# Optimization experiments

Measured on AMD Instinct MI355X. Metric: run time of the kernel, lower is better.

## Reference

```python
import jax, jax.numpy as jnp
import numpy as np

B, P, C = 64, 8732, 81
NEG_POS_RATIO = 3


def _smooth_l1_masked_sum(p, t, maskf):
    # smooth_l1 with beta=1, sum reduction, restricted to positive priors
    d = jnp.abs(p - t)
    l = jnp.where(d < 1.0, 0.5 * d * d, d - 0.5)  # [B,P,K]
    return jnp.sum(l.sum(-1) * maskf)


def setup_inputs() -> dict:
    key = jax.random.key(0)
    ks = jax.random.split(key, 6)
    loc_data = jax.random.normal(ks[0], (B, P, 4), jnp.float32)
    conf_data = jax.random.normal(ks[1], (B, P, C), jnp.float32)
    four_corners_data = jax.random.normal(ks[2], (B, P, 8), jnp.float32)
    loc_t = jax.random.normal(ks[3], (B, P, 4), jnp.float32)
    four_corners_t = jax.random.normal(ks[4], (B, P, 8), jnp.float32)
    conf_t = jax.random.randint(ks[5], (B, P), 0, C, jnp.int32)
    return {
        "loc_data": loc_data,
        "conf_data": conf_data,
        "four_corners_data": four_corners_data,
        "loc_t": loc_t,
        "four_corners_t": four_corners_t,
        "conf_t": conf_t,
    }


def reference(loc_data, conf_data, four_corners_data, loc_t, four_corners_t, conf_t):
    num_priors = conf_data.shape[1]
    pos = conf_t > 0                                  # [B,P]
    posf = pos.astype(conf_data.dtype)

    # localization + four-corner smooth-L1 over matched (positive) priors
    loss_l = _smooth_l1_masked_sum(loc_data, loc_t, posf)
    loss_four_corners = _smooth_l1_masked_sum(four_corners_data, four_corners_t, posf)

    # per-prior CE loss: log_sum_exp(conf) - conf[target]
    lse = jax.nn.logsumexp(conf_data, axis=-1)        # [B,P]
    gathered = jnp.take_along_axis(conf_data, conf_t[..., None], axis=-1)[..., 0]
    ce_all = lse - gathered                           # [B,P]

    # hard-negative mining: rank negatives by CE loss (double argsort)
    loss_c_mine = jnp.where(pos, 0.0, ce_all)
    loss_idx = jnp.argsort(-loss_c_mine, axis=1)      # descending sort indices
    idx_rank = jnp.argsort(loss_idx, axis=1)          # rank of each prior
    num_pos = pos.sum(axis=1, keepdims=True)          # [B,1]
    num_neg = jnp.minimum(NEG_POS_RATIO * num_pos, num_priors - 1)
    neg = idx_rank < num_neg                          # [B,P]

    sel = pos | neg
    loss_c = jnp.sum(jnp.where(sel, ce_all, 0.0))

    N = num_pos.sum().astype(conf_data.dtype)
    return (loss_l / N, loss_c / N, loss_four_corners / N)
```

## Files before the change

kernel.cpp:

```cpp
#include <hip/hip_runtime.h>


#define NB 64
#define NP 8732
#define NC 81
constexpr int BP = NB * NP;
constexpr int PBLK = (NP + 255) / 256;

__device__ inline float sl1(float d) {
    d = fabsf(d);
    return d < 1.0f ? 0.5f * d * d : d - 0.5f;
}

__global__ void k_init(float* acc_area) {
    if (threadIdx.x < 194) acc_area[threadIdx.x] = 0.0f;
}

__global__ __launch_bounds__(256) void k_main(
    const float* __restrict__ loc_data, const float* __restrict__ conf_data,
    const float* __restrict__ fc_data,  const float* __restrict__ loc_t,
    const float* __restrict__ fc_t,     const int* __restrict__ conf_t,
    float* __restrict__ ce, float* __restrict__ acc,
    int* __restrict__ npos_b, float* __restrict__ spos_b, float* __restrict__ sneg_b)
{
    const int b = blockIdx.y;
    const int t = threadIdx.x;
    const int p = (blockIdx.x << 8) + t;

    float l_sum = 0.0f, f_sum = 0.0f, sp = 0.0f, sn = 0.0f;
    int np = 0;

    if (p < NP) {
        const size_t g = (size_t)b * NP + p;
        const int tgt = conf_t[g];
        const float posf = (tgt > 0) ? 1.0f : 0.0f;
        np = (tgt > 0) ? 1 : 0;

        float4 a  = ((const float4*)loc_data)[g];
        float4 at = ((const float4*)loc_t)[g];
        l_sum = (sl1(a.x - at.x) + sl1(a.y - at.y) +
                 sl1(a.z - at.z) + sl1(a.w - at.w)) * posf;
        float4 c0 = ((const float4*)fc_data)[2 * g];
        float4 c1 = ((const float4*)fc_data)[2 * g + 1];
        float4 d0 = ((const float4*)fc_t)[2 * g];
        float4 d1 = ((const float4*)fc_t)[2 * g + 1];
        f_sum = (sl1(c0.x - d0.x) + sl1(c0.y - d0.y) + sl1(c0.z - d0.z) + sl1(c0.w - d0.w) +
                 sl1(c1.x - d1.x) + sl1(c1.y - d1.y) + sl1(c1.z - d1.z) + sl1(c1.w - d1.w)) * posf;

        const float* row = conf_data + g * NC;
        float s0 = 0.0f, s1 = 0.0f, s2 = 0.0f, s3 = 0.0f;
        #pragma unroll 5
        for (int c = 0; c < 80; c += 4) {
            s0 += __expf(row[c]);
            s1 += __expf(row[c + 1]);
            s2 += __expf(row[c + 2]);
            s3 += __expf(row[c + 3]);
        }
        float s = (s0 + s1) + (s2 + s3) + __expf(row[80]);
        float cev = __logf(s) - row[tgt];
        ce[g] = cev;
        sp = cev * posf;
        sn = cev - sp;
    }

    __shared__ float red[4][5];
    const int wave = t >> 6, lane = t & 63;
    float vnp = (float)np;
    #pragma unroll
    for (int o = 32; o; o >>= 1) {
        l_sum += __shfl_xor(l_sum, o, 64);
        f_sum += __shfl_xor(f_sum, o, 64);
        sp    += __shfl_xor(sp, o, 64);
        sn    += __shfl_xor(sn, o, 64);
        vnp   += __shfl_xor(vnp, o, 64);
    }
    if (lane == 0) {
        red[wave][0] = l_sum; red[wave][1] = f_sum;
        red[wave][2] = sp;    red[wave][3] = sn;   red[wave][4] = vnp;
    }
    __syncthreads();
    if (t == 0) {
        float rl = 0, rf = 0, rp = 0, rn = 0, rc = 0;
        #pragma unroll
        for (int w = 0; w < 4; ++w) {
            rl += red[w][0]; rf += red[w][1]; rp += red[w][2];
            rn += red[w][3]; rc += red[w][4];
        }
        atomicAdd(&acc[0], rl);
        atomicAdd(&acc[1], rf);
        atomicAdd(&spos_b[b], rp);
        atomicAdd(&sneg_b[b], rn);
        atomicAdd(&npos_b[b], (int)rc);
    }
}

__global__ __launch_bounds__(256) void k_batch(
    const float* __restrict__ ce, const int* __restrict__ conf_t,
    const int* __restrict__ npos_b, const float* __restrict__ spos_b,
    const float* __restrict__ sneg_b, float* __restrict__ loss_c_b)
{
    const int b = blockIdx.x;
    const int t = threadIdx.x;
    const int npos    = npos_b[b];
    const int nneg    = NP - npos;
    const int num_neg = min(3 * npos, NP - 1);

    if (num_neg >= nneg) {
        if (t == 0) loss_c_b[b] = spos_b[b] + sneg_b[b];
        return;
    }
    if (num_neg <= 0) {
        if (t == 0) loss_c_b[b] = spos_b[b];
        return;
    }

    __shared__ float ce_s[NP];
    __shared__ float sredf[4];
    __shared__ int   sredi[4];
    const float* crow = ce + (size_t)b * NP;
    const int*   trow = conf_t + (size_t)b * NP;
    for (int p = t; p < NP; p += 256)
        ce_s[p] = (trow[p] > 0) ? -1.0f : crow[p];
    __syncthreads();

    const int wave = t >> 6, lane = t & 63;
    const int K = num_neg;
    unsigned lo = 0u, hi = 0x7f800000u;
    while (lo < hi) {
        unsigned mid = lo + ((hi - lo) >> 1);
        float v = __uint_as_float(mid);
        int c_t = 0;
        for (int p = t; p < NP; p += 256) c_t += (ce_s[p] > v) ? 1 : 0;
        #pragma unroll
        for (int o = 32; o; o >>= 1) c_t += __shfl_xor(c_t, o, 64);
        __syncthreads();
        if (lane == 0) sredi[wave] = c_t;
        __syncthreads();
        int cnt = sredi[0] + sredi[1] + sredi[2] + sredi[3];
        if (cnt < K) hi = mid; else lo = mid + 1;
    }
    float v = __uint_as_float(lo);
    int c_t = 0; float s_t = 0.0f;
    for (int p = t; p < NP; p += 256) {
        float x = ce_s[p];
        if (x > v) { c_t++; s_t += x; }
    }
    #pragma unroll
    for (int o = 32; o; o >>= 1) {
        c_t += __shfl_xor(c_t, o, 64);
        s_t += __shfl_xor(s_t, o, 64);
    }
    __syncthreads();
    if (lane == 0) { sredi[wave] = c_t; sredf[wave] = s_t; }
    __syncthreads();
    if (t == 0) {
        int   cnt = sredi[0] + sredi[1] + sredi[2] + sredi[3];
        float sgt = sredf[0] + sredf[1] + sredf[2] + sredf[3];
        loss_c_b[b] = spos_b[b] + sgt + (float)(K - cnt) * v;
    }
}

__global__ void k_final(const float* __restrict__ acc,
                        const float* __restrict__ loss_c_b,
                        const int* __restrict__ npos_b,
                        float* __restrict__ out)
{
    const int t = threadIdx.x;
    float lc = loss_c_b[t];
    int   np = npos_b[t];
    #pragma unroll
    for (int o = 32; o; o >>= 1) {
        lc += __shfl_xor(lc, o, 64);
        np += __shfl_xor(np, o, 64);
    }
    if (t == 0) {
        float N = (float)np;
        out[0] = acc[0] / N;
        out[1] = lc / N;
        out[2] = acc[1] / N;
    }
}

extern "C" void kernel_launch(void* const* d_in, const int* in_sizes, int n_in,
                              void* d_out, int out_size, void* d_ws, size_t ws_size,
                              hipStream_t stream)
{
    const float* loc_data  = (const float*)d_in[0];
    const float* conf_data = (const float*)d_in[1];
    const float* fc_data   = (const float*)d_in[2];
    const float* loc_t     = (const float*)d_in[3];
    const float* fc_t      = (const float*)d_in[4];
    const int*   conf_t    = (const int*)d_in[5];
    float* out = (float*)d_out;

    float* ce       = (float*)d_ws;
    float* acc      = ce + BP;
    int*   npos_b   = (int*)(acc + 2);
    float* spos_b   = (float*)(npos_b + 64);
    float* sneg_b   = spos_b + 64;
    float* loss_c_b = sneg_b + 64;

    hipLaunchKernelGGL(k_init,  dim3(1), dim3(256), 0, stream, acc);
    hipLaunchKernelGGL(k_main,  dim3(PBLK, NB), dim3(256), 0, stream,
                       loc_data, conf_data, fc_data, loc_t, fc_t, conf_t,
                       ce, acc, npos_b, spos_b, sneg_b);
    hipLaunchKernelGGL(k_batch, dim3(NB), dim3(256), 0, stream,
                       ce, conf_t, npos_b, spos_b, sneg_b, loss_c_b);
    hipLaunchKernelGGL(k_final, dim3(1), dim3(64), 0, stream,
                       acc, loss_c_b, npos_b, out);
}
```

Measured before the change: 315.4 us.

## Stage conf rows in shared memory with coalesced loads, four threads per row

New measurement: 479.2 us. 51.9% more time.

```diff
diff --git a/kernel.cpp b/kernel.cpp
--- a/kernel.cpp
+++ b/kernel.cpp
@@ -4,8 +4,9 @@
 #define NB 64
 #define NP 8732
 #define NC 81
-constexpr int BP = NB * NP;
-constexpr int PBLK = (NP + 255) / 256;
+constexpr int BP   = NB * NP;
+constexpr int ROWS = 64;
+constexpr int TPB  = (NP + ROWS - 1) / ROWS;
 
 __device__ inline float sl1(float d) {
     d = fabsf(d);
@@ -23,19 +24,29 @@
     float* __restrict__ ce, float* __restrict__ acc,
     int* __restrict__ npos_b, float* __restrict__ spos_b, float* __restrict__ sneg_b)
 {
-    const int b = blockIdx.y;
-    const int t = threadIdx.x;
-    const int p = (blockIdx.x << 8) + t;
-
-    float l_sum = 0.0f, f_sum = 0.0f, sp = 0.0f, sn = 0.0f;
+    __shared__ float conf_s[ROWS * NC];
+    __shared__ int   tgt_s[ROWS];
+    __shared__ float red[4][5];
+
+    const int b    = blockIdx.y;
+    const int r0   = blockIdx.x * ROWS;
+    const int nrows = min(ROWS, NP - r0);
+    const int t    = threadIdx.x;
+    const size_t rowbase = (size_t)b * NP + r0;
+
+    const int nf4 = (nrows * NC) >> 2;
+    const float4* src = (const float4*)(conf_data + rowbase * NC);
+    for (int i = t; i < nf4; i += 256)
+        ((float4*)conf_s)[i] = src[i];
+
+    float l_sum = 0.0f, f_sum = 0.0f;
     int np = 0;
-
-    if (p < NP) {
-        const size_t g = (size_t)b * NP + p;
+    if (t < nrows) {
+        const size_t g = rowbase + t;
         const int tgt = conf_t[g];
+        tgt_s[t] = tgt;
         const float posf = (tgt > 0) ? 1.0f : 0.0f;
         np = (tgt > 0) ? 1 : 0;
-
         float4 a  = ((const float4*)loc_data)[g];
         float4 at = ((const float4*)loc_t)[g];
         l_sum = (sl1(a.x - at.x) + sl1(a.y - at.y) +
@@ -46,24 +57,28 @@
         float4 d1 = ((const float4*)fc_t)[2 * g + 1];
         f_sum = (sl1(c0.x - d0.x) + sl1(c0.y - d0.y) + sl1(c0.z - d0.z) + sl1(c0.w - d0.w) +
                  sl1(c1.x - d1.x) + sl1(c1.y - d1.y) + sl1(c1.z - d1.z) + sl1(c1.w - d1.w)) * posf;
-
-        const float* row = conf_data + g * NC;
-        float s0 = 0.0f, s1 = 0.0f, s2 = 0.0f, s3 = 0.0f;
+    }
+    __syncthreads();
+
+    float sp = 0.0f, sn = 0.0f;
+    const int r = t >> 2, q = t & 3;
+    if (r < nrows) {
+        const float* rowp = conf_s + r * NC;
+        const int c0 = q * 20;
+        const int c1 = (q == 3) ? NC : c0 + 20;
+        float s = 0.0f;
         #pragma unroll 5
-        for (int c = 0; c < 80; c += 4) {
-            s0 += __expf(row[c]);
-            s1 += __expf(row[c + 1]);
-            s2 += __expf(row[c + 2]);
-            s3 += __expf(row[c + 3]);
+        for (int c = c0; c < c1; ++c) s += __expf(rowp[c]);
+        s += __shfl_xor(s, 1, 64);
+        s += __shfl_xor(s, 2, 64);
+        if (q == 0) {
+            const int tgt = tgt_s[r];
+            const float cev = __logf(s) - rowp[tgt];
+            ce[rowbase + r] = cev;
+            if (tgt > 0) sp = cev; else sn = cev;
         }
-        float s = (s0 + s1) + (s2 + s3) + __expf(row[80]);
-        float cev = __logf(s) - row[tgt];
-        ce[g] = cev;
-        sp = cev * posf;
-        sn = cev - sp;
-    }
-
-    __shared__ float red[4][5];
+    }
+
     const int wave = t >> 6, lane = t & 63;
     float vnp = (float)np;
     #pragma unroll
@@ -201,7 +216,7 @@
     float* loss_c_b = sneg_b + 64;
 
     hipLaunchKernelGGL(k_init,  dim3(1), dim3(256), 0, stream, acc);
-    hipLaunchKernelGGL(k_main,  dim3(PBLK, NB), dim3(256), 0, stream,
+    hipLaunchKernelGGL(k_main,  dim3(TPB, NB), dim3(256), 0, stream,
                        loc_data, conf_data, fc_data, loc_t, fc_t, conf_t,
                        ce, acc, npos_b, spos_b, sneg_b);
     hipLaunchKernelGGL(k_batch, dim3(NB), dim3(256), 0, stream,
```

## Vectorize conf row loads with float4 pairs and spread atomics over slots

Applied to the files above, without the earlier changes.

Measured after the change: 322.0 us. 1.02x slower.

```diff
diff --git a/kernel.cpp b/kernel.cpp
--- a/kernel.cpp
+++ b/kernel.cpp
@@ -4,104 +4,132 @@
 #define NB 64
 #define NP 8732
 #define NC 81
-constexpr int BP = NB * NP;
-constexpr int PBLK = (NP + 255) / 256;
+constexpr int BP   = NB * NP;
+constexpr int NQ   = BP / 4;
+constexpr int NT   = NQ * 2;
+constexpr int NBLK = NT / 64;
+constexpr int QPB  = NP / 4;
 
 __device__ inline float sl1(float d) {
     d = fabsf(d);
     return d < 1.0f ? 0.5f * d * d : d - 0.5f;
 }
-
-__global__ void k_init(float* acc_area) {
-    if (threadIdx.x < 194) acc_area[threadIdx.x] = 0.0f;
-}
-
-__global__ __launch_bounds__(256) void k_main(
+__device__ inline float e4(float4 v) {
+    return __expf(v.x) + __expf(v.y) + __expf(v.z) + __expf(v.w);
+}
+
+__global__ void k_init(float* z) {
+    z[threadIdx.x] = 0.0f;
+}
+
+__global__ __launch_bounds__(64) void k_main(
     const float* __restrict__ loc_data, const float* __restrict__ conf_data,
     const float* __restrict__ fc_data,  const float* __restrict__ loc_t,
     const float* __restrict__ fc_t,     const int* __restrict__ conf_t,
     float* __restrict__ ce, float* __restrict__ acc,
-    int* __restrict__ npos_b, float* __restrict__ spos_b, float* __restrict__ sneg_b)
-{
-    const int b = blockIdx.y;
-    const int t = threadIdx.x;
-    const int p = (blockIdx.x << 8) + t;
-
-    float l_sum = 0.0f, f_sum = 0.0f, sp = 0.0f, sn = 0.0f;
-    int np = 0;
-
-    if (p < NP) {
-        const size_t g = (size_t)b * NP + p;
-        const int tgt = conf_t[g];
-        const float posf = (tgt > 0) ? 1.0f : 0.0f;
-        np = (tgt > 0) ? 1 : 0;
-
-        float4 a  = ((const float4*)loc_data)[g];
-        float4 at = ((const float4*)loc_t)[g];
-        l_sum = (sl1(a.x - at.x) + sl1(a.y - at.y) +
-                 sl1(a.z - at.z) + sl1(a.w - at.w)) * posf;
-        float4 c0 = ((const float4*)fc_data)[2 * g];
-        float4 c1 = ((const float4*)fc_data)[2 * g + 1];
-        float4 d0 = ((const float4*)fc_t)[2 * g];
-        float4 d1 = ((const float4*)fc_t)[2 * g + 1];
-        f_sum = (sl1(c0.x - d0.x) + sl1(c0.y - d0.y) + sl1(c0.z - d0.z) + sl1(c0.w - d0.w) +
-                 sl1(c1.x - d1.x) + sl1(c1.y - d1.y) + sl1(c1.z - d1.z) + sl1(c1.w - d1.w)) * posf;
-
-        const float* row = conf_data + g * NC;
-        float s0 = 0.0f, s1 = 0.0f, s2 = 0.0f, s3 = 0.0f;
-        #pragma unroll 5
-        for (int c = 0; c < 80; c += 4) {
-            s0 += __expf(row[c]);
-            s1 += __expf(row[c + 1]);
-            s2 += __expf(row[c + 2]);
-            s3 += __expf(row[c + 3]);
+    float* __restrict__ spos_b, float* __restrict__ sneg_b, float* __restrict__ npf_b)
+{
+    const int lane = threadIdx.x;
+    const int tid  = blockIdx.x * 64 + lane;
+    const int q    = tid >> 1;
+    const int h    = tid & 1;
+
+    const float4* cf = (const float4*)conf_data + (size_t)q * 81;
+    float s0 = 0.f, s1 = 0.f, s2 = 0.f, s3 = 0.f;
+    if (h == 0) {
+        float4 v;
+        #pragma unroll 10
+        for (int k = 0; k < 20; ++k) { v = cf[k]; s0 += e4(v); }
+        v = cf[20];
+        s0 += __expf(v.x); s1 += __expf(v.y) + __expf(v.z) + __expf(v.w);
+        #pragma unroll 10
+        for (int k = 21; k < 40; ++k) { v = cf[k]; s1 += e4(v); }
+        v = cf[40];
+        s1 += __expf(v.x) + __expf(v.y); s2 += __expf(v.z) + __expf(v.w);
+    } else {
+        float4 v;
+        #pragma unroll 10
+        for (int k = 41; k < 60; ++k) { v = cf[k]; s2 += e4(v); }
+        v = cf[60];
+        s2 += __expf(v.x) + __expf(v.y) + __expf(v.z); s3 += __expf(v.w);
+        #pragma unroll 10
+        for (int k = 61; k < 81; ++k) { v = cf[k]; s3 += e4(v); }
+    }
+    s0 += __shfl_xor(s0, 1, 64);
+    s1 += __shfl_xor(s1, 1, 64);
+    s2 += __shfl_xor(s2, 1, 64);
+    s3 += __shfl_xor(s3, 1, 64);
+
+    const size_t rA = (size_t)4 * q + 2 * h;
+    const int2 tg = *(const int2*)(conf_t + rA);
+    const float sA = h ? s2 : s0;
+    const float sB = h ? s3 : s1;
+    const float ceA = __logf(sA) - conf_data[rA * NC + tg.x];
+    const float ceB = __logf(sB) - conf_data[(rA + 1) * NC + tg.y];
+    *(float2*)(ce + rA) = make_float2(ceA, ceB);
+    float sp = (tg.x > 0 ? ceA : 0.f) + (tg.y > 0 ? ceB : 0.f);
+    float sn = (ceA + ceB) - sp;
+    float np = (float)((tg.x > 0) + (tg.y > 0));
+
+    float l_acc = 0.f, f_acc = 0.f;
+    #pragma unroll
+    for (int j = 0; j < 2; ++j) {
+        const int i = tid + j * NT;
+        float4 a = ((const float4*)loc_data)[i];
+        float4 b = ((const float4*)loc_t)[i];
+        float m = (conf_t[i] > 0) ? 1.f : 0.f;
+        l_acc += m * (sl1(a.x - b.x) + sl1(a.y - b.y) + sl1(a.z - b.z) + sl1(a.w - b.w));
+    }
+    #pragma unroll
+    for (int j = 0; j < 4; ++j) {
+        const int i = tid + j * NT;
+        float4 a = ((const float4*)fc_data)[i];
+        float4 b = ((const float4*)fc_t)[i];
+        float m = (conf_t[i >> 1] > 0) ? 1.f : 0.f;
+        f_acc += m * (sl1(a.x - b.x) + sl1(a.y - b.y) + sl1(a.z - b.z) + sl1(a.w - b.w));
+    }
+
+    const int b_ = q / QPB;
+    const int b0 = __shfl(b_, 0, 64);
+    const int bL = __shfl(b_, 63, 64);
+    const float m0 = (b_ == b0) ? 1.f : 0.f;
+    float sp0 = sp * m0, sp1 = sp - sp0;
+    float sn0 = sn * m0, sn1 = sn - sn0;
+    float np0 = np * m0, np1 = np - np0;
+    #pragma unroll
+    for (int o = 32; o; o >>= 1) {
+        l_acc += __shfl_xor(l_acc, o, 64);
+        f_acc += __shfl_xor(f_acc, o, 64);
+        sp0 += __shfl_xor(sp0, o, 64);
+        sp1 += __shfl_xor(sp1, o, 64);
+        sn0 += __shfl_xor(sn0, o, 64);
+        sn1 += __shfl_xor(sn1, o, 64);
+        np0 += __shfl_xor(np0, o, 64);
+        np1 += __shfl_xor(np1, o, 64);
+    }
+    if (lane == 0) {
+        const int slot = blockIdx.x & 31;
+        atomicAdd(&acc[slot],      l_acc);
+        atomicAdd(&acc[32 + slot], f_acc);
+        atomicAdd(&spos_b[b0], sp0);
+        atomicAdd(&sneg_b[b0], sn0);
+        atomicAdd(&npf_b[b0],  np0);
+        if (bL != b0) {
+            atomicAdd(&spos_b[bL], sp1);
+            atomicAdd(&sneg_b[bL], sn1);
+            atomicAdd(&npf_b[bL],  np1);
         }
-        float s = (s0 + s1) + (s2 + s3) + __expf(row[80]);
-        float cev = __logf(s) - row[tgt];
-        ce[g] = cev;
-        sp = cev * posf;
-        sn = cev - sp;
-    }
-
-    __shared__ float red[4][5];
-    const int wave = t >> 6, lane = t & 63;
-    float vnp = (float)np;
-    #pragma unroll
-    for (int o = 32; o; o >>= 1) {
-        l_sum += __shfl_xor(l_sum, o, 64);
-        f_sum += __shfl_xor(f_sum, o, 64);
-        sp    += __shfl_xor(sp, o, 64);
-        sn    += __shfl_xor(sn, o, 64);
-        vnp   += __shfl_xor(vnp, o, 64);
-    }
-    if (lane == 0) {
-        red[wave][0] = l_sum; red[wave][1] = f_sum;
-        red[wave][2] = sp;    red[wave][3] = sn;   red[wave][4] = vnp;
-    }
-    __syncthreads();
-    if (t == 0) {
-        float rl = 0, rf = 0, rp = 0, rn = 0, rc = 0;
-        #pragma unroll
-        for (int w = 0; w < 4; ++w) {
-            rl += red[w][0]; rf += red[w][1]; rp += red[w][2];
-            rn += red[w][3]; rc += red[w][4];
-        }
-        atomicAdd(&acc[0], rl);
-        atomicAdd(&acc[1], rf);
-        atomicAdd(&spos_b[b], rp);
-        atomicAdd(&sneg_b[b], rn);
-        atomicAdd(&npos_b[b], (int)rc);
     }
 }
 
 __global__ __launch_bounds__(256) void k_batch(
     const float* __restrict__ ce, const int* __restrict__ conf_t,
-    const int* __restrict__ npos_b, const float* __restrict__ spos_b,
+    const float* __restrict__ npf_b, const float* __restrict__ spos_b,
     const float* __restrict__ sneg_b, float* __restrict__ loss_c_b)
 {
     const int b = blockIdx.x;
     const int t = threadIdx.x;
-    const int npos    = npos_b[b];
+    const int npos    = (int)(npf_b[b] + 0.5f);
     const int nneg    = NP - npos;
     const int num_neg = min(3 * npos, NP - 1);
 
@@ -162,22 +190,26 @@
 
 __global__ void k_final(const float* __restrict__ acc,
                         const float* __restrict__ loss_c_b,
-                        const int* __restrict__ npos_b,
+                        const float* __restrict__ npf_b,
                         float* __restrict__ out)
 {
     const int t = threadIdx.x;
+    const float av = acc[t];
+    float a0 = (t < 32) ? av : 0.0f;
+    float a1 = av - a0;
     float lc = loss_c_b[t];
-    int   np = npos_b[t];
+    float np = npf_b[t];
     #pragma unroll
     for (int o = 32; o; o >>= 1) {
+        a0 += __shfl_xor(a0, o, 64);
+        a1 += __shfl_xor(a1, o, 64);
         lc += __shfl_xor(lc, o, 64);
         np += __shfl_xor(np, o, 64);
     }
     if (t == 0) {
-        float N = (float)np;
-        out[0] = acc[0] / N;
-        out[1] = lc / N;
-        out[2] = acc[1] / N;
+        out[0] = a0 / np;
+        out[1] = lc / np;
+        out[2] = a1 / np;
     }
 }
 
@@ -195,17 +227,17 @@
 
     float* ce       = (float*)d_ws;
     float* acc      = ce + BP;
-    int*   npos_b   = (int*)(acc + 2);
-    float* spos_b   = (float*)(npos_b + 64);
+    float* spos_b   = acc + 64;
     float* sneg_b   = spos_b + 64;
-    float* loss_c_b = sneg_b + 64;
-
-    hipLaunchKernelGGL(k_init,  dim3(1), dim3(256), 0, stream, acc);
-    hipLaunchKernelGGL(k_main,  dim3(PBLK, NB), dim3(256), 0, stream,
+    float* npf_b    = sneg_b + 64;
+    float* loss_c_b = npf_b + 64;
+
+    hipLaunchKernelGGL(k_init,  dim3(1),    dim3(256), 0, stream, acc);
+    hipLaunchKernelGGL(k_main,  dim3(NBLK), dim3(64),  0, stream,
                        loc_data, conf_data, fc_data, loc_t, fc_t, conf_t,
-                       ce, acc, npos_b, spos_b, sneg_b);
-    hipLaunchKernelGGL(k_batch, dim3(NB), dim3(256), 0, stream,
-                       ce, conf_t, npos_b, spos_b, sneg_b, loss_c_b);
-    hipLaunchKernelGGL(k_final, dim3(1), dim3(64), 0, stream,
-                       acc, loss_c_b, npos_b, out);
-}
+                       ce, acc, spos_b, sneg_b, npf_b);
+    hipLaunchKernelGGL(k_batch, dim3(NB),   dim3(256), 0, stream,
+                       ce, conf_t, npf_b, spos_b, sneg_b, loss_c_b);
+    hipLaunchKernelGGL(k_final, dim3(1),    dim3(64),  0, stream,
+                       acc, loss_c_b, npf_b, out);
+}
```
